# Performance work log

Measured on AMD Instinct MI355X. Metric: run time of the kernel, lower is better.

Reference implementation:

```python
import jax, jax.numpy as jnp
import numpy as np
import math

HEADS = 16
SPH = 64      # size_per_head
KEY = 64      # key_size (defaults to size_per_head)
EMB = 1024
STEP = 3


def extract_seq_patches(x, kernel_size, step):
    # x: [B, L, D] -> [B, L, kernel_size, D]; patch j at pos t is x_pad[t - p_left + j*step]
    B, L, D = x.shape
    k_size = kernel_size + (step - 1) * (kernel_size - 1)
    p_right = (k_size - 1) // 2
    p_left = k_size - 1 - p_right
    xp = jnp.pad(x, ((0, 0), (p_left, p_right), (0, 0)))
    xs = [xp[:, i:i + L] for i in range(0, k_size, step)]  # kernel_size slices
    return jnp.stack(xs, axis=2)


def setup_inputs() -> dict:
    key = jax.random.key(0)
    kx, kq, kk, kv = jax.random.split(key, 4)
    B, L = 2, 4096
    x = jax.random.normal(kx, (B, L, EMB), dtype=jnp.float32)
    W_q = jax.random.normal(kq, (EMB, HEADS * KEY), dtype=jnp.float32) * 0.02
    W_k = jax.random.normal(kk, (EMB, HEADS * KEY), dtype=jnp.float32) * 0.02
    W_v = jax.random.normal(kv, (EMB, HEADS * SPH), dtype=jnp.float32) * 0.02
    return {"x": x, "W_q": W_q, "W_k": W_k, "W_v": W_v}


def _forward(x, W_q, W_k, W_v):
    B, L, D = x.shape
    pad_len = STEP - L % STEP
    x = jnp.pad(x, ((0, 0), (0, pad_len), (0, 0)))
    new_len = L + pad_len
    blocks = new_len // STEP
    q = x @ W_q  # [B, new_len, H*KEY]
    k = x @ W_k
    v = x @ W_v
    ksz = 1 + 2 * (STEP - 1)  # kernel_size = 5
    kp = extract_seq_patches(k, ksz, STEP)  # [B, new_len, ksz, H*KEY]
    vp = extract_seq_patches(v, ksz, STEP)
    # reshape to [B, H, step, blocks, d]
    q = q.reshape(B, blocks, STEP, HEADS, KEY).transpose(0, 3, 2, 1, 4)
    kb = k.reshape(B, blocks, STEP, HEADS, KEY).transpose(0, 3, 2, 1, 4)
    vb = v.reshape(B, blocks, STEP, HEADS, SPH).transpose(0, 3, 2, 1, 4)
    # neighbor patches: [B, H, step, blocks, ksz, d]
    kp = kp.reshape(B, blocks, STEP, ksz, HEADS, KEY).transpose(0, 4, 2, 1, 3, 5)
    vp = vp.reshape(B, blocks, STEP, ksz, HEADS, SPH).transpose(0, 4, 2, 1, 3, 5)
    scale = 1.0 / math.sqrt(KEY)
    # strided attention over blocks (same residue mod step): [B,H,step,blocks,blocks]
    a = jnp.einsum('bhsqk,bhspk->bhsqp', q, kb) * scale
    # block-local neighbor attention: [B,H,step,blocks,ksz]
    ap = jnp.einsum('bhsqk,bhsqnk->bhsqn', q, kp) * scale
    A = jax.nn.softmax(jnp.concatenate([a, ap], axis=-1), axis=-1)
    a, ap = A[..., :blocks], A[..., blocks:]
    o = (jnp.einsum('bhsqp,bhspd->bhsqd', a, vb)
         + jnp.einsum('bhsqn,bhsqnd->bhsqd', ap, vp))
    o = o.transpose(0, 3, 2, 1, 4).reshape(B, new_len, HEADS * SPH)
    return o[:, :L]


def reference(x, W_q, W_k, W_v):
    return _forward(x, W_q, W_k, W_v)
```

## Files before the change

### kernel.cpp

```cpp
#include <hip/hip_runtime.h>
#include <hip/hip_bf16.h>

typedef unsigned int u32;
typedef unsigned short u16;
typedef short s8v __attribute__((ext_vector_type(8)));
typedef short s4v __attribute__((ext_vector_type(4)));
typedef float f4v __attribute__((ext_vector_type(4)));
typedef float f16v __attribute__((ext_vector_type(16)));
typedef u32 u32x2 __attribute__((ext_vector_type(2)));
typedef u32 u32x4 __attribute__((ext_vector_type(4)));

#define NBLK 1366
#define VROW 1376
#define QSCALE 0.18033688011112042f

__device__ __forceinline__ u16 f2b(float f) {
  u32 u = __builtin_bit_cast(u32, f);
  u = (u + 0x7FFFu + ((u >> 16) & 1u)) >> 16;
  return (u16)u;
}

__device__ __forceinline__ u32 cvtpk(float a, float b) {
  u32 r;
  asm("v_cvt_pk_bf16_f32 %0, %1, %2" : "=v"(r) : "v"(a), "v"(b));
  return r;
}

__device__ __forceinline__ float fexp2(float x) {
#if defined(__has_builtin)
#if __has_builtin(__builtin_amdgcn_exp2f)
  return __builtin_amdgcn_exp2f(x);
#define FEXP2_DONE 1
#endif
#endif
#ifndef FEXP2_DONE
  float r;
  asm("v_exp_f32 %0, %1" : "=v"(r) : "v"(x));
  return r;
#endif
}

__device__ __forceinline__ void gll16(const void* g, void* l) {
  __builtin_amdgcn_global_load_lds(
      (const __attribute__((address_space(1))) u32*)g,
      (__attribute__((address_space(3))) u32*)l, 16, 0, 0);
}

__device__ __forceinline__ f4v mfma32(s8v a, s8v b, f4v c) {
  return __builtin_amdgcn_mfma_f32_16x16x32_bf16(a, b, c, 0, 0, 0);
}

__device__ __forceinline__ f16v mfma3216(s8v a, s8v b, f16v c) {
  return __builtin_amdgcn_mfma_f32_32x32x16_bf16(a, b, c, 0, 0, 0);
}

__device__ __forceinline__ s4v lo4(s8v v) {
  return __builtin_shufflevector(v, v, 0, 1, 2, 3);
}
__device__ __forceinline__ s4v hi4(s8v v) {
  return __builtin_shufflevector(v, v, 4, 5, 6, 7);
}

__global__ __launch_bounds__(256) void k_prep(const float* __restrict__ x,
                                              const float* __restrict__ Wq,
                                              const float* __restrict__ Wk,
                                              const float* __restrict__ Wv,
                                              u16* __restrict__ xb,
                                              u16* __restrict__ Wt,
                                              u16* __restrict__ Vt) {
  const int bid = blockIdx.x;
  const int tid = threadIdx.x;
  if (bid < 4160) {
    long base = ((long)bid * 256 + tid) * 8;
    if (base >= 8320L * 1024L) return;
    int m = (int)(base >> 10);
    int c = (int)(base & 1023);
    int b = m / 4098;
    int t = m - b * 4098;
    s8v pack;
    if (m < 8196 && t < 4096) {
      const float* src = x + ((size_t)b * 4096 + t) * 1024 + c;
      float4 v0 = *(const float4*)(src);
      float4 v1 = *(const float4*)(src + 4);
      pack[0] = (short)f2b(v0.x); pack[1] = (short)f2b(v0.y);
      pack[2] = (short)f2b(v0.z); pack[3] = (short)f2b(v0.w);
      pack[4] = (short)f2b(v1.x); pack[5] = (short)f2b(v1.y);
      pack[6] = (short)f2b(v1.z); pack[7] = (short)f2b(v1.w);
    } else {
#pragma unroll
      for (int i = 0; i < 8; ++i) pack[i] = 0;
    }
    *(s8v*)(xb + base) = pack;
  } else if (bid < 7232) {
    __shared__ float tile[32][33];
    int bid3 = bid - 4160;
    int z = bid3 >> 10;
    int rem = bid3 & 1023;
    const float* W = (z == 0) ? Wq : ((z == 1) ? Wk : Wv);
    u16* dst = Wt + (size_t)z * 1024 * 1024;
    int n0 = (rem & 31) * 32, k0 = (rem >> 5) * 32;
    int tx = tid & 31, ty = tid >> 5;
#pragma unroll
    for (int i = 0; i < 4; ++i)
      tile[ty + i * 8][tx] = W[(size_t)(k0 + ty + i * 8) * 1024 + n0 + tx];
    __syncthreads();
#pragma unroll
    for (int i = 0; i < 4; ++i)
      dst[(size_t)(n0 + ty + i * 8) * 1024 + k0 + tx] = f2b(tile[tx][ty + i * 8]);
  } else {
    int gidx = (bid - 7232) * 256 + tid;
    if (gidx < 6144) {
      u16* dst = Vt + (size_t)gidx * VROW + NBLK;
#pragma unroll
      for (int i = 0; i < 10; ++i) dst[i] = 0;
    } else if (gidx < 6400) {
      Vt[(size_t)6144 * VROW + (gidx - 6144)] = 0;
    }
  }
}

__global__ __launch_bounds__(256) void k_gemm_qkv(const u16* __restrict__ xb,
                                                  const u16* __restrict__ Wt,
                                                  u16* __restrict__ Qp,
                                                  u16* __restrict__ Kp,
                                                  u16* __restrict__ Vt) {
  const int zid = blockIdx.z;
  const int m0 = blockIdx.x * 128;
  const int n0 = blockIdx.y * 128;
  const u16* Bg = Wt + (size_t)zid * 1024 * 1024 + (size_t)n0 * 1024;

  __shared__ __align__(16) u16 shl[16384];
  u16* A0 = shl;
  u16* A1 = shl + 4096;
  u16* B0 = shl + 8192;
  u16* B1 = shl + 12288;

  const int tid = threadIdx.x;
  const int lane = tid & 63;
  const int w = tid >> 6;
  const int wr = w >> 1, wc = w & 1;
  const int lo = lane & 15, g = lane >> 4;

  const int lrow = lane >> 2;
  const int csrc = (lane & 3) ^ ((lane >> 3) & 3);
  const int rsw = (g ^ ((lo >> 1) & 3)) << 4;

  f4v acc[4][4];
#pragma unroll
  for (int i = 0; i < 4; ++i)
#pragma unroll
    for (int j = 0; j < 4; ++j) {
      f4v z = {0.f, 0.f, 0.f, 0.f};
      acc[i][j] = z;
    }

  auto stage = [&](int kt, u16* Ab, u16* Bb) {
#pragma unroll
    for (int c = 0; c < 2; ++c) {
      int rloc = w * 32 + c * 16 + lrow;
      gll16(xb + (size_t)(m0 + rloc) * 1024 + kt + csrc * 8,
            Ab + (w * 32 + c * 16) * 32);
      gll16(Bg + (size_t)rloc * 1024 + kt + csrc * 8,
            Bb + (w * 32 + c * 16) * 32);
    }
  };

  auto compute = [&](const u16* Ab, const u16* Bb) {
    s8v af[4], bf[4];
#pragma unroll
    for (int i = 0; i < 4; ++i) {
      int ar = wr * 64 + i * 16 + lo;
      af[i] = *(const s8v*)((const char*)Ab + ar * 64 + rsw);
      int br = wc * 64 + i * 16 + lo;
      bf[i] = *(const s8v*)((const char*)Bb + br * 64 + rsw);
    }
    __builtin_amdgcn_s_setprio(1);
#pragma unroll
    for (int i = 0; i < 4; ++i)
#pragma unroll
      for (int j = 0; j < 4; ++j)
        acc[i][j] = mfma32(af[i], bf[j], acc[i][j]);
    __builtin_amdgcn_s_setprio(0);
  };

#define BAR_VM4                                             \
  asm volatile("s_waitcnt vmcnt(4)" ::: "memory");          \
  __builtin_amdgcn_s_barrier();                             \
  asm volatile("" ::: "memory");
#define BAR_LGKM                                            \
  asm volatile("s_waitcnt lgkmcnt(0)" ::: "memory");        \
  __builtin_amdgcn_s_barrier();                             \
  asm volatile("" ::: "memory");

  stage(0, A0, B0);
#pragma unroll 1
  for (int kk = 0; kk < 15; ++kk) {
    int kt = kk * 64;
    stage(kt + 32, A1, B1);
    BAR_VM4
    compute(A0, B0);
    BAR_LGKM
    stage(kt + 64, A0, B0);
    BAR_VM4
    compute(A1, B1);
    BAR_LGKM
  }
  stage(31 * 32, A1, B1);
  BAR_VM4
  compute(A0, B0);
  BAR_LGKM
  asm volatile("s_waitcnt vmcnt(0)" ::: "memory");
  __builtin_amdgcn_s_barrier();
  asm volatile("" ::: "memory");
  compute(A1, B1);
  __syncthreads();

#undef BAR_VM4
#undef BAR_LGKM

  const float esc = (zid == 0) ? QSCALE : 1.0f;
  if (zid != 2) {
    u16* dq = (zid == 0) ? Qp : Kp;
#pragma unroll
    for (int i = 0; i < 4; ++i) {
#pragma unroll
      for (int r = 0; r < 4; ++r) {
        int m = m0 + wr * 64 + i * 16 + g * 4 + r;
        if (m >= 8196) continue;
        int b = m / 4098;
        int t = m - b * 4098;
        int s = t % 3;
        int p = t / 3;
        int cb = (b * 3 + s) * 16;
#pragma unroll
        for (int j = 0; j < 4; ++j) {
          int n = n0 + wc * 64 + j * 16 + lo;
          int h = n >> 6, d = n & 63;
          dq[(size_t)((cb + h) * NBLK + p) * 64 + d] = f2b(acc[i][j][r] * esc);
        }
      }
    }
  } else {
    u16* tile = shl;
#pragma unroll
    for (int i = 0; i < 4; ++i)
#pragma unroll
      for (int r = 0; r < 4; ++r) {
        int ml = wr * 64 + i * 16 + g * 4 + r;
#pragma unroll
        for (int j = 0; j < 4; ++j) {
          int nl = wc * 64 + j * 16 + lo;
          tile[ml * 128 + nl] = f2b(acc[i][j][r]);
        }
      }
    __syncthreads();
    for (int pair = tid; pair < 384; pair += 256) {
      int nl = pair & 127;
      int s = pair >> 7;
      int n = n0 + nl;
      int h = n >> 6, d = n & 63;
      for (int b = 0; b < 2; ++b) {
        int mlo = m0 > b * 4098 ? m0 : b * 4098;
        int cap = b * 4098 + 4096;
        int mhi = (m0 + 128 < cap) ? m0 + 128 : cap;
        if (mlo >= mhi) continue;
        int t_lo = mlo - b * 4098;
        int add = (s - (t_lo % 3) + 3) % 3;
        int t = t_lo + add;
        int tend = mhi - b * 4098;
        u16* dst = Vt + (size_t)(((b * 3 + s) * 16 + h) * 64 + d) * VROW;
        for (; t < tend; t += 3)
          dst[t / 3] = tile[(b * 4098 + t - m0) * 128 + nl];
      }
    }
  }
}

__global__ __launch_bounds__(256, 4) void k_attn(const u16* __restrict__ Qp,
                                                 const u16* __restrict__ Kp,
                                                 const u16* __restrict__ Vt,
                                                 float* __restrict__ out) {
  const int wg = blockIdx.x;
  const int idx = (wg & 7) * 132 + (wg >> 3);
  const int combo = idx / 11;
  const int qb = idx - combo * 11;
  const int b = combo / 48;
  const int rem = combo - b * 48;
  const int s = rem >> 4;
  const int h = rem & 15;
  const int tid = threadIdx.x, lane = tid & 63, w = tid >> 6;
  const int lq = lane & 31, lh = lane >> 5;

  const u16* Qg = Qp + (size_t)combo * (NBLK * 64);
  const u16* Kg = Kp + (size_t)combo * (NBLK * 64);
  const u16* Vg = Vt + (size_t)combo * (64 * VROW);

  __shared__ __align__(16) u16 att[2][4][64 * 36];

  const int qg = qb * 128 + w * 32 + lq;
  const int qc = (qg < NBLK) ? qg : (NBLK - 1);
  s8v qf[4];
#pragma unroll
  for (int ss = 0; ss < 4; ++ss)
    qf[ss] = *(const s8v*)(Qg + (size_t)qc * 64 + ss * 16 + lh * 8);

  f16v oacc0, oacc1;
#pragma unroll
  for (int i = 0; i < 16; ++i) { oacc0[i] = 0.f; oacc1[i] = 0.f; }
  float dpart[4] = {0.f, 0.f, 0.f, 0.f};

  const int srow = tid >> 2;
  const int sch = (tid & 3) * 2;
  const int ssub = (tid & 3) * 8;
  s8v kr0, kr1, vr0, vr1;

  auto load_regs = [&](int jt) {
    const int j0 = jt * 64;
    const u16* kp = Kg + (size_t)(j0 + srow) * 64 + sch * 8;
    kr0 = *(const s8v*)(kp);
    kr1 = *(const s8v*)(kp + 8);
    const u16* vp = Vg + (size_t)srow * VROW + j0 + sch * 8;
    vr0 = *(const s8v*)(vp);
    vr1 = *(const s8v*)(vp + 8);
  };

  auto stage_write = [&](int slot) {
    u16* K0 = att[slot][0];
    u16* K1 = att[slot][1];
    u16* V0 = att[slot][2];
    u16* V1 = att[slot][3];
    const int kb = srow * 36 + ssub;
    *(s4v*)(K0 + kb) = lo4(kr0);
    *(s4v*)(K0 + kb + 4) = hi4(kr0);
    *(s4v*)(K1 + kb) = lo4(kr1);
    *(s4v*)(K1 + kb + 4) = hi4(kr1);
    const int vb0 = srow * 36 + sch * 4;
    *(s4v*)(V0 + vb0) = lo4(vr0);
    *(s4v*)(V1 + vb0) = hi4(vr0);
    *(s4v*)(V0 + vb0 + 4) = lo4(vr1);
    *(s4v*)(V1 + vb0 + 4) = hi4(vr1);
  };

  const int qmin = qb * 128;

  auto compute = [&](int slot, int jt) {
    const int j0 = jt * 64;
    const u16* Kb = att[slot][lh];
    const u16* Vl0 = att[slot][2];
    const u16* Vl1 = att[slot][3];

    const bool special = ((j0 <= qmin + 130) && (j0 + 65 >= qmin)) || (j0 + 64 > NBLK);
#pragma unroll
    for (int jb = 0; jb < 2; ++jb) {
      f16v sacc;
#pragma unroll
      for (int i = 0; i < 16; ++i) sacc[i] = 0.f;
      __builtin_amdgcn_s_setprio(1);
#pragma unroll
      for (int ss = 0; ss < 4; ++ss) {
        const u16* kp = Kb + (jb * 32 + lq) * 36 + ss * 8;
        s4v a = *(const s4v*)kp;
        s4v b2 = *(const s4v*)(kp + 4);
        s8v kf = __builtin_shufflevector(a, b2, 0, 1, 2, 3, 4, 5, 6, 7);
        sacc = mfma3216(kf, qf[ss], sacc);
      }
      __builtin_amdgcn_s_setprio(0);

      float e[16];
      if (special) {
#pragma unroll
        for (int r = 0; r < 16; ++r) {
          int j = j0 + jb * 32 + (r & 3) + 8 * (r >> 2) + 4 * lh;
          float ev = fexp2(sacc[r]);
          int dd = j - qg;
          float fac = (j < NBLK) ? (((dd <= 2) && (dd >= -2)) ? 2.f : 1.f) : 0.f;
          e[r] = ev * fac;
        }
      } else {
#pragma unroll
        for (int r = 0; r < 16; ++r) e[r] = fexp2(sacc[r]);
      }
#pragma unroll
      for (int r = 0; r < 16; ++r) dpart[r & 3] += e[r];

#pragma unroll
      for (int g2 = 0; g2 < 2; ++g2) {
        u32 pe0 = cvtpk(e[g2 * 8 + 0], e[g2 * 8 + 1]);
        u32 pe1 = cvtpk(e[g2 * 8 + 2], e[g2 * 8 + 3]);
        u32 pe2 = cvtpk(e[g2 * 8 + 4], e[g2 * 8 + 5]);
        u32 pe3 = cvtpk(e[g2 * 8 + 6], e[g2 * 8 + 7]);
        asm("v_permlane32_swap_b32 %0, %1" : "+v"(pe0), "+v"(pe2));
        asm("v_permlane32_swap_b32 %0, %1" : "+v"(pe1), "+v"(pe3));
        u32x4 fw;
        fw[0] = pe0; fw[1] = pe1; fw[2] = pe2; fw[3] = pe3;
        s8v ef8 = __builtin_bit_cast(s8v, fw);
        const int ci = (jb * 4 + g2 * 2 + lh) * 4;
        s4v v0a = *(const s4v*)(Vl0 + lq * 36 + ci);
        s4v v0b = *(const s4v*)(Vl1 + lq * 36 + ci);
        s8v vf0 = __builtin_shufflevector(v0a, v0b, 0, 1, 2, 3, 4, 5, 6, 7);
        s4v v1a = *(const s4v*)(Vl0 + (32 + lq) * 36 + ci);
        s4v v1b = *(const s4v*)(Vl1 + (32 + lq) * 36 + ci);
        s8v vf1 = __builtin_shufflevector(v1a, v1b, 0, 1, 2, 3, 4, 5, 6, 7);
        __builtin_amdgcn_s_setprio(1);
        oacc0 = mfma3216(ef8, vf0, oacc0);
        oacc1 = mfma3216(ef8, vf1, oacc1);
        __builtin_amdgcn_s_setprio(0);
      }
    }
  };

#define LGKM_BAR                                            \
  asm volatile("s_waitcnt lgkmcnt(0)" ::: "memory");        \
  __builtin_amdgcn_s_barrier();                             \
  asm volatile("" ::: "memory");

  load_regs(0);
  stage_write(0);
  load_regs(1);
  LGKM_BAR

#pragma unroll 1
  for (int t = 0; t < 21; ++t) {
    compute(t & 1, t);
    stage_write((t + 1) & 1);
    if (t < 20) load_regs(t + 2);
    LGKM_BAR
  }
  compute(1, 21);

#undef LGKM_BAR

  float dtot = (dpart[0] + dpart[1]) + (dpart[2] + dpart[3]);
  dtot += __shfl_xor(dtot, 32, 64);

  const int hbase = h * 64;
#pragma unroll
  for (int r = 0; r < 16; ++r) {
    int cr = (r & 3) + 8 * (r >> 2) + 4 * lh;
    int q = qb * 128 + w * 32 + cr;
    float dq = __shfl(dtot, cr, 64);
    dq += (q == 0 || q == NBLK - 1) ? 2.f : ((q == 1 || q == NBLK - 2) ? 1.f : 0.f);
    float rr = 1.f / dq;
    int t = 3 * q + s;
    if (q < NBLK && t < 4096) {
      float* orow = out + ((size_t)b * 4096 + t) * 1024 + hbase + lq;
      orow[0] = oacc0[r] * rr;
      orow[32] = oacc1[r] * rr;
    }
  }
}

extern "C" void kernel_launch(void* const* d_in, const int* in_sizes, int n_in,
                              void* d_out, int out_size, void* d_ws, size_t ws_size,
                              hipStream_t stream) {
  const float* x  = (const float*)d_in[0];
  const float* Wq = (const float*)d_in[1];
  const float* Wk = (const float*)d_in[2];
  const float* Wv = (const float*)d_in[3];
  float* out = (float*)d_out;

  u16* ws = (u16*)d_ws;
  u16* xb = ws;
  u16* Wt = xb + 8519680;
  u16* Qp = Wt + 3145728;
  u16* Kp = Qp + 8392704;
  u16* Vt = Kp + 8392704;

  k_prep<<<dim3(7257), 256, 0, stream>>>(x, Wq, Wk, Wv, xb, Wt, Vt);
  k_gemm_qkv<<<dim3(65, 8, 3), 256, 0, stream>>>(xb, Wt, Qp, Kp, Vt);
  k_attn<<<dim3(1056), 256, 0, stream>>>(Qp, Kp, Vt, out);
}
```

Measured before the change: 207.9 us.

## Process two query tiles per wave in attention to reuse staged K/V

Each wave now handles 64 queries (two 32-row MFMA tiles) instead of 32, so every K/V tile staged in shared memory feeds twice the MFMA work. The workgroup count drops from 1056 to 576 and launch bounds fall from 4 to 2 waves per SIMD to make room for the doubled accumulators. The aim is to cut K/V global loads and LDS traffic per unit of compute. The cost is higher register pressure, lower occupancy and fewer workgroups to spread across the CUs.

Result: slower. 215.8 us (+3.8%).

```diff
diff --git a/kernel.cpp b/kernel.cpp
--- a/kernel.cpp
+++ b/kernel.cpp
@@ -276,14 +276,14 @@
   }
 }
 
-__global__ __launch_bounds__(256, 4) void k_attn(const u16* __restrict__ Qp,
+__global__ __launch_bounds__(256, 2) void k_attn(const u16* __restrict__ Qp,
                                                  const u16* __restrict__ Kp,
                                                  const u16* __restrict__ Vt,
                                                  float* __restrict__ out) {
   const int wg = blockIdx.x;
-  const int idx = (wg & 7) * 132 + (wg >> 3);
-  const int combo = idx / 11;
-  const int qb = idx - combo * 11;
+  const int idx = (wg & 7) * 72 + (wg >> 3);
+  const int combo = idx / 6;
+  const int qb = idx - combo * 6;
   const int b = combo / 48;
   const int rem = combo - b * 48;
   const int s = rem >> 4;
@@ -297,17 +297,22 @@
 
   __shared__ __align__(16) u16 att[2][4][64 * 36];
 
-  const int qg = qb * 128 + w * 32 + lq;
-  const int qc = (qg < NBLK) ? qg : (NBLK - 1);
-  s8v qf[4];
-#pragma unroll
-  for (int ss = 0; ss < 4; ++ss)
-    qf[ss] = *(const s8v*)(Qg + (size_t)qc * 64 + ss * 16 + lh * 8);
-
-  f16v oacc0, oacc1;
-#pragma unroll
-  for (int i = 0; i < 16; ++i) { oacc0[i] = 0.f; oacc1[i] = 0.f; }
-  float dpart[4] = {0.f, 0.f, 0.f, 0.f};
+  const int qbase = qb * 256 + w * 64;
+  const int qgA = qbase + lq;
+  const int qgB = qbase + 32 + lq;
+  const int qcA = (qgA < NBLK) ? qgA : (NBLK - 1);
+  const int qcB = (qgB < NBLK) ? qgB : (NBLK - 1);
+  s8v qfA[4], qfB[4];
+#pragma unroll
+  for (int ss = 0; ss < 4; ++ss) {
+    qfA[ss] = *(const s8v*)(Qg + (size_t)qcA * 64 + ss * 16 + lh * 8);
+    qfB[ss] = *(const s8v*)(Qg + (size_t)qcB * 64 + ss * 16 + lh * 8);
+  }
+
+  f16v oA0, oA1, oB0, oB1;
+#pragma unroll
+  for (int i = 0; i < 16; ++i) { oA0[i] = 0.f; oA1[i] = 0.f; oB0[i] = 0.f; oB1[i] = 0.f; }
+  float dpA0 = 0.f, dpA1 = 0.f, dpB0 = 0.f, dpB1 = 0.f;
 
   const int srow = tid >> 2;
   const int sch = (tid & 3) * 2;
@@ -341,7 +346,7 @@
     *(s4v*)(V1 + vb0 + 4) = hi4(vr1);
   };
 
-  const int qmin = qb * 128;
+  const int qmin = qb * 256;
 
   auto compute = [&](int slot, int jt) {
     const int j0 = jt * 64;
@@ -349,12 +354,12 @@
     const u16* Vl0 = att[slot][2];
     const u16* Vl1 = att[slot][3];
 
-    const bool special = ((j0 <= qmin + 130) && (j0 + 65 >= qmin)) || (j0 + 64 > NBLK);
+    const bool special = ((j0 <= qmin + 258) && (j0 + 66 >= qmin)) || (j0 + 64 > NBLK);
 #pragma unroll
     for (int jb = 0; jb < 2; ++jb) {
-      f16v sacc;
-#pragma unroll
-      for (int i = 0; i < 16; ++i) sacc[i] = 0.f;
+      f16v saccA, saccB;
+#pragma unroll
+      for (int i = 0; i < 16; ++i) { saccA[i] = 0.f; saccB[i] = 0.f; }
       __builtin_amdgcn_s_setprio(1);
 #pragma unroll
       for (int ss = 0; ss < 4; ++ss) {
@@ -362,38 +367,57 @@
         s4v a = *(const s4v*)kp;
         s4v b2 = *(const s4v*)(kp + 4);
         s8v kf = __builtin_shufflevector(a, b2, 0, 1, 2, 3, 4, 5, 6, 7);
-        sacc = mfma3216(kf, qf[ss], sacc);
+        saccA = mfma3216(kf, qfA[ss], saccA);
+        saccB = mfma3216(kf, qfB[ss], saccB);
       }
       __builtin_amdgcn_s_setprio(0);
 
-      float e[16];
+      float eA[16], eB[16];
       if (special) {
 #pragma unroll
         for (int r = 0; r < 16; ++r) {
           int j = j0 + jb * 32 + (r & 3) + 8 * (r >> 2) + 4 * lh;
-          float ev = fexp2(sacc[r]);
-          int dd = j - qg;
-          float fac = (j < NBLK) ? (((dd <= 2) && (dd >= -2)) ? 2.f : 1.f) : 0.f;
-          e[r] = ev * fac;
+          float evA = fexp2(saccA[r]);
+          float evB = fexp2(saccB[r]);
+          int ddA = j - qgA;
+          int ddB = j - qgB;
+          float inb = (j < NBLK) ? 1.f : 0.f;
+          float facA = ((ddA <= 2) && (ddA >= -2)) ? 2.f : 1.f;
+          float facB = ((ddB <= 2) && (ddB >= -2)) ? 2.f : 1.f;
+          eA[r] = evA * facA * inb;
+          eB[r] = evB * facB * inb;
         }
       } else {
 #pragma unroll
-        for (int r = 0; r < 16; ++r) e[r] = fexp2(sacc[r]);
-      }
-#pragma unroll
-      for (int r = 0; r < 16; ++r) dpart[r & 3] += e[r];
+        for (int r = 0; r < 16; ++r) { eA[r] = fexp2(saccA[r]); eB[r] = fexp2(saccB[r]); }
+      }
+#pragma unroll
+      for (int r = 0; r < 16; r += 2) {
+        dpA0 += eA[r]; dpA1 += eA[r + 1];
+        dpB0 += eB[r]; dpB1 += eB[r + 1];
+      }
 
 #pragma unroll
       for (int g2 = 0; g2 < 2; ++g2) {
-        u32 pe0 = cvtpk(e[g2 * 8 + 0], e[g2 * 8 + 1]);
-        u32 pe1 = cvtpk(e[g2 * 8 + 2], e[g2 * 8 + 3]);
-        u32 pe2 = cvtpk(e[g2 * 8 + 4], e[g2 * 8 + 5]);
-        u32 pe3 = cvtpk(e[g2 * 8 + 6], e[g2 * 8 + 7]);
-        asm("v_permlane32_swap_b32 %0, %1" : "+v"(pe0), "+v"(pe2));
-        asm("v_permlane32_swap_b32 %0, %1" : "+v"(pe1), "+v"(pe3));
-        u32x4 fw;
-        fw[0] = pe0; fw[1] = pe1; fw[2] = pe2; fw[3] = pe3;
-        s8v ef8 = __builtin_bit_cast(s8v, fw);
+        u32 pa0 = cvtpk(eA[g2 * 8 + 0], eA[g2 * 8 + 1]);
+        u32 pa1 = cvtpk(eA[g2 * 8 + 2], eA[g2 * 8 + 3]);
+        u32 pa2 = cvtpk(eA[g2 * 8 + 4], eA[g2 * 8 + 5]);
+        u32 pa3 = cvtpk(eA[g2 * 8 + 6], eA[g2 * 8 + 7]);
+        asm("v_permlane32_swap_b32 %0, %1" : "+v"(pa0), "+v"(pa2));
+        asm("v_permlane32_swap_b32 %0, %1" : "+v"(pa1), "+v"(pa3));
+        u32x4 fwA;
+        fwA[0] = pa0; fwA[1] = pa1; fwA[2] = pa2; fwA[3] = pa3;
+        s8v efA8 = __builtin_bit_cast(s8v, fwA);
+        u32 pb0 = cvtpk(eB[g2 * 8 + 0], eB[g2 * 8 + 1]);
+        u32 pb1 = cvtpk(eB[g2 * 8 + 2], eB[g2 * 8 + 3]);
+        u32 pb2 = cvtpk(eB[g2 * 8 + 4], eB[g2 * 8 + 5]);
+        u32 pb3 = cvtpk(eB[g2 * 8 + 6], eB[g2 * 8 + 7]);
+        asm("v_permlane32_swap_b32 %0, %1" : "+v"(pb0), "+v"(pb2));
+        asm("v_permlane32_swap_b32 %0, %1" : "+v"(pb1), "+v"(pb3));
+        u32x4 fwB;
+        fwB[0] = pb0; fwB[1] = pb1; fwB[2] = pb2; fwB[3] = pb3;
+        s8v efB8 = __builtin_bit_cast(s8v, fwB);
+
         const int ci = (jb * 4 + g2 * 2 + lh) * 4;
         s4v v0a = *(const s4v*)(Vl0 + lq * 36 + ci);
         s4v v0b = *(const s4v*)(Vl1 + lq * 36 + ci);
@@ -402,8 +426,10 @@
         s4v v1b = *(const s4v*)(Vl1 + (32 + lq) * 36 + ci);
         s8v vf1 = __builtin_shufflevector(v1a, v1b, 0, 1, 2, 3, 4, 5, 6, 7);
         __builtin_amdgcn_s_setprio(1);
-        oacc0 = mfma3216(ef8, vf0, oacc0);
-        oacc1 = mfma3216(ef8, vf1, oacc1);
+        oA0 = mfma3216(efA8, vf0, oA0);
+        oA1 = mfma3216(efA8, vf1, oA1);
+        oB0 = mfma3216(efB8, vf0, oB0);
+        oB1 = mfma3216(efB8, vf1, oB1);
         __builtin_amdgcn_s_setprio(0);
       }
     }
@@ -430,22 +456,38 @@
 
 #undef LGKM_BAR
 
-  float dtot = (dpart[0] + dpart[1]) + (dpart[2] + dpart[3]);
-  dtot += __shfl_xor(dtot, 32, 64);
+  float dtA = (dpA0 + dpA1);
+  float dtB = (dpB0 + dpB1);
+  dtA += __shfl_xor(dtA, 32, 64);
+  dtB += __shfl_xor(dtB, 32, 64);
 
   const int hbase = h * 64;
 #pragma unroll
   for (int r = 0; r < 16; ++r) {
     int cr = (r & 3) + 8 * (r >> 2) + 4 * lh;
-    int q = qb * 128 + w * 32 + cr;
-    float dq = __shfl(dtot, cr, 64);
-    dq += (q == 0 || q == NBLK - 1) ? 2.f : ((q == 1 || q == NBLK - 2) ? 1.f : 0.f);
-    float rr = 1.f / dq;
-    int t = 3 * q + s;
-    if (q < NBLK && t < 4096) {
-      float* orow = out + ((size_t)b * 4096 + t) * 1024 + hbase + lq;
-      orow[0] = oacc0[r] * rr;
-      orow[32] = oacc1[r] * rr;
+    {
+      int q = qbase + cr;
+      float dq = __shfl(dtA, cr, 64);
+      dq += (q == 0 || q == NBLK - 1) ? 2.f : ((q == 1 || q == NBLK - 2) ? 1.f : 0.f);
+      float rr = 1.f / dq;
+      int t = 3 * q + s;
+      if (q < NBLK && t < 4096) {
+        float* orow = out + ((size_t)b * 4096 + t) * 1024 + hbase + lq;
+        orow[0] = oA0[r] * rr;
+        orow[32] = oA1[r] * rr;
+      }
+    }
+    {
+      int q = qbase + 32 + cr;
+      float dq = __shfl(dtB, cr, 64);
+      dq += (q == 0 || q == NBLK - 1) ? 2.f : ((q == 1 || q == NBLK - 2) ? 1.f : 0.f);
+      float rr = 1.f / dq;
+      int t = 3 * q + s;
+      if (q < NBLK && t < 4096) {
+        float* orow = out + ((size_t)b * 4096 + t) * 1024 + hbase + lq;
+        orow[0] = oB0[r] * rr;
+        orow[32] = oB1[r] * rr;
+      }
     }
   }
 }
@@ -468,5 +510,5 @@
 
   k_prep<<<dim3(7257), 256, 0, stream>>>(x, Wq, Wk, Wv, xb, Wt, Vt);
   k_gemm_qkv<<<dim3(65, 8, 3), 256, 0, stream>>>(xb, Wt, Qp, Kp, Vt);
-  k_attn<<<dim3(1056), 256, 0, stream>>>(Qp, Kp, Vt, out);
-}
+  k_attn<<<dim3(576), 256, 0, stream>>>(Qp, Kp, Vt, out);
+}
```
